# Optimization experiments

Measured on AMD Instinct MI355X. Metric: run time of the kernel, lower is better.

The kernel has to match this reference:

```python
import jax, jax.numpy as jnp
import numpy as np

B, C, CI, H, W = 8, 256, 128, 48, 48


def conv1x1(x, w, b):
    # x: (B,C,H,W), w: (CI,C), b: (CI,)
    return jnp.einsum('bchw,oc->bohw', x, w) + b[None, :, None, None]


def setup_inputs() -> dict:
    key = jax.random.key(0)
    ks = jax.random.split(key, 14)
    s = 1.0 / np.sqrt(C)
    d = {
        'x_1': jax.random.normal(ks[0], (B, C, H, W), jnp.float32),
        'x_2': jax.random.normal(ks[1], (B, C, H, W), jnp.float32),
    }
    names = ['v1', 'k1', 'q1', 'v2', 'k2', 'q2']
    for i, n in enumerate(names):
        d['w_' + n] = jax.random.uniform(ks[2 + 2 * i], (CI, C), jnp.float32, -s, s)
        d['b_' + n] = jax.random.uniform(ks[3 + 2 * i], (CI,), jnp.float32, -s, s)
    return d


def reference(x_1, x_2, w_v1, b_v1, w_k1, b_k1, w_q1, b_q1,
              w_v2, b_v2, w_k2, b_k2, w_q2, b_q2):
    b, ci, h, w = x_1.shape[0], w_v1.shape[0], x_1.shape[2], x_1.shape[3]
    n = h * w
    V1 = conv1x1(x_1, w_v1, b_v1).reshape(b, ci, n)
    K1 = conv1x1(x_1, w_k1, b_k1).reshape(b, ci, n)
    Q1 = conv1x1(x_1, w_q1, b_q1).reshape(b, ci, n)
    V2 = conv1x1(x_2, w_v2, b_v2).reshape(b, ci, n)
    K2 = conv1x1(x_2, w_k2, b_k2).reshape(b, ci, n)
    Q2 = conv1x1(x_2, w_q2, b_q2).reshape(b, ci, n)
    # sigmoid-gated cross attention, (B, N, N)
    R12 = jax.nn.sigmoid(jnp.einsum('bcn,bcm->bnm', Q1, K2))
    R21 = jax.nn.sigmoid(jnp.einsum('bcn,bcm->bnm', Q2, K1))
    Fu1 = jnp.einsum('bnm,bcm->bcn', R12, V2).reshape(b, ci, h, w)
    Fu2 = jnp.einsum('bnm,bcm->bcn', R21, V1).reshape(b, ci, h, w)
    y_1 = jnp.concatenate([x_1, Fu1], axis=1)
    y_2 = jnp.concatenate([x_2, Fu2], axis=1)
    return (y_1, y_2)
```

## Files before the change

kernel.cpp:

```cpp
#include <hip/hip_runtime.h>
#include <hip/hip_bf16.h>


typedef __bf16 bf16;
typedef __bf16 bf16x8 __attribute__((ext_vector_type(8)));
typedef __bf16 bf16x4 __attribute__((ext_vector_type(4)));
typedef float f32x4 __attribute__((ext_vector_type(4)));
typedef float f32x16 __attribute__((ext_vector_type(16)));
typedef unsigned int u32x4 __attribute__((ext_vector_type(4)));

#define NB 8
#define NC 256
#define NCI 128
#define NHW 2304
#define NT32 72

__global__ __launch_bounds__(256) void wconv_kernel(
    const float* __restrict__ w0, const float* __restrict__ w1,
    const float* __restrict__ w2, const float* __restrict__ w3,
    const float* __restrict__ w4, const float* __restrict__ w5,
    bf16* __restrict__ dst)
{
    int idx = (blockIdx.x * 256 + threadIdx.x) * 8;
    int m = idx >> 15;
    int off = idx & 32767;
    const float* w = (m == 0) ? w0 : (m == 1) ? w1 : (m == 2) ? w2
                   : (m == 3) ? w3 : (m == 4) ? w4 : w5;
    f32x4 a0 = *(const f32x4*)(w + off);
    f32x4 a1 = *(const f32x4*)(w + off + 4);
    bf16x8 o;
    #pragma unroll
    for (int j = 0; j < 4; ++j) { o[j] = (bf16)a0[j]; o[4 + j] = (bf16)a1[j]; }
    *(bf16x8*)(dst + idx) = o;
}

__global__ __launch_bounds__(256) void qkv_kernel(
    const float* __restrict__ x1, const float* __restrict__ x2,
    const bf16* __restrict__ wb,
    const float* __restrict__ bv1, const float* __restrict__ bk1, const float* __restrict__ bq1,
    const float* __restrict__ bv2, const float* __restrict__ bk2, const float* __restrict__ bq2,
    bf16* __restrict__ Qt, bf16* __restrict__ Kt, bf16* __restrict__ Vt,
    float* __restrict__ out)
{
    __shared__ __align__(16) bf16 Xt[32 * 264];

    int gid = blockIdx.x;
    int nt = gid % NT32;
    int s = (gid / NT32) & 1;
    int b = gid / (2 * NT32);
    int n0 = nt * 32;

    const float* x = s ? x2 : x1;
    const bf16* wv = wb + (size_t)(s * 3 + 0) * (NCI * NC);
    const bf16* wk = wb + (size_t)(s * 3 + 1) * (NCI * NC);
    const bf16* wq = wb + (size_t)(s * 3 + 2) * (NCI * NC);
    const float* bv = s ? bv2 : bv1;
    const float* bk = s ? bk2 : bk1;
    const float* bq = s ? bq2 : bq1;
    float* outy = out + (size_t)s * (NB * 384 * NHW);

    int tid = threadIdx.x;
    {
        int n_off = (tid & 3) * 8;
        int c0l = tid >> 2;
        #pragma unroll
        for (int i = 0; i < 4; ++i) {
            int c = c0l + i * 64;
            const float* src = x + ((size_t)(b * NC + c) * NHW + n0 + n_off);
            f32x4 a0 = *(const f32x4*)src;
            f32x4 a1 = *(const f32x4*)(src + 4);
            float* dsty = outy + ((size_t)(b * 384 + c) * NHW + n0 + n_off);
            *(f32x4*)dsty = a0;
            *(f32x4*)(dsty + 4) = a1;
            #pragma unroll
            for (int j = 0; j < 4; ++j) {
                Xt[(n_off + j) * 264 + c] = (bf16)a0[j];
                Xt[(n_off + 4 + j) * 264 + c] = (bf16)a1[j];
            }
        }
    }
    __syncthreads();

    int lane = tid & 63;
    int wid = tid >> 6;
    int row = lane & 15, quad = lane >> 4;
    int ci_base = wid * 32;

    f32x4 acc[3][2][2];
    #pragma unroll
    for (int t = 0; t < 3; ++t)
        #pragma unroll
        for (int mi = 0; mi < 2; ++mi)
            #pragma unroll
            for (int j = 0; j < 2; ++j)
                acc[t][mi][j] = (f32x4){0.f, 0.f, 0.f, 0.f};

    const bf16* wptr[3] = {wq, wk, wv};
    #pragma unroll
    for (int ks = 0; ks < 8; ++ks) {
        int c0 = ks * 32 + quad * 8;
        bf16x8 bfrag[2];
        #pragma unroll
        for (int j = 0; j < 2; ++j)
            bfrag[j] = *(const bf16x8*)&Xt[(j * 16 + row) * 264 + c0];
        #pragma unroll
        for (int t = 0; t < 3; ++t) {
            #pragma unroll
            for (int mi = 0; mi < 2; ++mi) {
                bf16x8 afrag = *(const bf16x8*)&wptr[t][(size_t)(ci_base + mi * 16 + row) * NC + c0];
                #pragma unroll
                for (int j = 0; j < 2; ++j)
                    acc[t][mi][j] = __builtin_amdgcn_mfma_f32_16x16x32_bf16(
                        afrag, bfrag[j], acc[t][mi][j], 0, 0, 0);
            }
        }
    }

    size_t qkbase = ((size_t)s * NB + b) * NHW * NCI;
    size_t vbase  = ((size_t)s * NB + b) * NCI * NHW;
    #pragma unroll
    for (int mi = 0; mi < 2; ++mi) {
        int ci0 = ci_base + mi * 16 + quad * 4;
        f32x4 bq4 = *(const f32x4*)&bq[ci0];
        f32x4 bk4 = *(const f32x4*)&bk[ci0];
        f32x4 bv4 = *(const f32x4*)&bv[ci0];
        #pragma unroll
        for (int j = 0; j < 2; ++j) {
            int n = n0 + j * 16 + row;
            bf16x4 pk;
            #pragma unroll
            for (int r = 0; r < 4; ++r) pk[r] = (bf16)(acc[0][mi][j][r] + bq4[r]);
            *(bf16x4*)&Qt[qkbase + (size_t)n * NCI + ci0] = pk;
            #pragma unroll
            for (int r = 0; r < 4; ++r) pk[r] = (bf16)(acc[1][mi][j][r] + bk4[r]);
            *(bf16x4*)&Kt[qkbase + (size_t)n * NCI + ci0] = pk;
            #pragma unroll
            for (int r = 0; r < 4; ++r)
                Vt[vbase + (size_t)(nt * 128 + ci0 + r) * 32 + (j * 16 + row)] =
                    (bf16)(acc[2][mi][j][r] + bv4[r]);
        }
    }
}

__global__ __launch_bounds__(256, 3) void attn_kernel(
    const bf16* __restrict__ Qt, const bf16* __restrict__ Kt, const bf16* __restrict__ Vt,
    float* __restrict__ out)
{
    __shared__ __align__(16) float RED[8192];

    int gid = blockIdx.x;
    int b = gid & 7;
    int dir = (gid >> 3) & 1;
    int nt = gid >> 4;

    int tid = threadIdx.x;
    int lane = tid & 63;
    int mq = tid >> 6;
    int col = lane & 31, hi = lane >> 5;

    int sq = dir, skv = dir ^ 1;
    const bf16* q = Qt + ((size_t)sq  * NB + b) * (NHW * NCI);
    const bf16* k = Kt + ((size_t)skv * NB + b) * (NHW * NCI);
    const bf16* v = Vt + ((size_t)skv * NB + b) * (NCI * NHW);
    float* outy = out + (size_t)dir * (NB * 384 * NHW) + ((size_t)b * 384 + 256) * NHW;

    int nw = nt * 32;

    bf16x8 qf[8];
    #pragma unroll
    for (int j = 0; j < 8; ++j)
        qf[j] = *(const bf16x8*)&q[(size_t)(nw + col) * NCI + j * 16 + hi * 8];

    f32x16 o0, o1, o2, o3;
    #pragma unroll
    for (int j = 0; j < 16; ++j) { o0[j] = 0.f; o1[j] = 0.f; o2[j] = 0.f; o3[j] = 0.f; }

    for (int i = 0; i < 18; ++i) {
        int m0 = mq * 576 + i * 32;
        const bf16* kp = k + (size_t)(m0 + col) * NCI + hi * 8;

        f32x16 s;
        #pragma unroll
        for (int j = 0; j < 16; ++j) s[j] = 0.f;
        __builtin_amdgcn_s_setprio(1);
        #pragma unroll
        for (int j = 0; j < 8; ++j) {
            bf16x8 kf = *(const bf16x8*)(kp + j * 16);
            s = __builtin_amdgcn_mfma_f32_32x32x16_bf16(kf, qf[j], s, 0, 0, 0);
        }
        __builtin_amdgcn_s_setprio(0);

        #pragma unroll
        for (int r = 0; r < 16; ++r) {
            float e = __expf(-s[r]);
            s[r] = __builtin_amdgcn_rcpf(1.0f + e);
        }
        u32x4 pbw0, pbw1;
        {
            unsigned int a0, a1, c0, c1;
            asm("v_cvt_pk_bf16_f32 %0, %1, %2" : "=v"(a0) : "v"(s[0]), "v"(s[1]));
            asm("v_cvt_pk_bf16_f32 %0, %1, %2" : "=v"(a1) : "v"(s[2]), "v"(s[3]));
            asm("v_cvt_pk_bf16_f32 %0, %1, %2" : "=v"(c0) : "v"(s[4]), "v"(s[5]));
            asm("v_cvt_pk_bf16_f32 %0, %1, %2" : "=v"(c1) : "v"(s[6]), "v"(s[7]));
            asm volatile("v_permlane32_swap_b32 %0, %1" : "+v"(a0), "+v"(c0));
            asm volatile("v_permlane32_swap_b32 %0, %1" : "+v"(a1), "+v"(c1));
            pbw0 = (u32x4){a0, a1, c0, c1};
        }
        {
            unsigned int a0, a1, c0, c1;
            asm("v_cvt_pk_bf16_f32 %0, %1, %2" : "=v"(a0) : "v"(s[8]),  "v"(s[9]));
            asm("v_cvt_pk_bf16_f32 %0, %1, %2" : "=v"(a1) : "v"(s[10]), "v"(s[11]));
            asm("v_cvt_pk_bf16_f32 %0, %1, %2" : "=v"(c0) : "v"(s[12]), "v"(s[13]));
            asm("v_cvt_pk_bf16_f32 %0, %1, %2" : "=v"(c1) : "v"(s[14]), "v"(s[15]));
            asm volatile("v_permlane32_swap_b32 %0, %1" : "+v"(a0), "+v"(c0));
            asm volatile("v_permlane32_swap_b32 %0, %1" : "+v"(a1), "+v"(c1));
            pbw1 = (u32x4){a0, a1, c0, c1};
        }

        const bf16* vp = v + ((size_t)(mq * 18 + i) * 128 + col) * 32 + hi * 8;
        __builtin_amdgcn_s_setprio(1);
        {
            bf16x8 pf = __builtin_bit_cast(bf16x8, pbw0);
            o0 = __builtin_amdgcn_mfma_f32_32x32x16_bf16(*(const bf16x8*)(vp + 0*1024), pf, o0, 0, 0, 0);
            o1 = __builtin_amdgcn_mfma_f32_32x32x16_bf16(*(const bf16x8*)(vp + 1*1024), pf, o1, 0, 0, 0);
            o2 = __builtin_amdgcn_mfma_f32_32x32x16_bf16(*(const bf16x8*)(vp + 2*1024), pf, o2, 0, 0, 0);
            o3 = __builtin_amdgcn_mfma_f32_32x32x16_bf16(*(const bf16x8*)(vp + 3*1024), pf, o3, 0, 0, 0);
        }
        {
            bf16x8 pf = __builtin_bit_cast(bf16x8, pbw1);
            o0 = __builtin_amdgcn_mfma_f32_32x32x16_bf16(*(const bf16x8*)(vp + 0*1024 + 16), pf, o0, 0, 0, 0);
            o1 = __builtin_amdgcn_mfma_f32_32x32x16_bf16(*(const bf16x8*)(vp + 1*1024 + 16), pf, o1, 0, 0, 0);
            o2 = __builtin_amdgcn_mfma_f32_32x32x16_bf16(*(const bf16x8*)(vp + 2*1024 + 16), pf, o2, 0, 0, 0);
            o3 = __builtin_amdgcn_mfma_f32_32x32x16_bf16(*(const bf16x8*)(vp + 3*1024 + 16), pf, o3, 0, 0, 0);
        }
        __builtin_amdgcn_s_setprio(0);
    }

    float* buf0 = RED;
    float* buf1 = RED + 4096;

    auto wpart = [&](float* buf, const f32x16& a, int cb) {
        #pragma unroll
        for (int g = 0; g < 4; ++g) {
            f32x4 v4;
            #pragma unroll
            for (int j = 0; j < 4; ++j) v4[j] = a[g * 4 + j];
            *(f32x4*)&buf[lane * 64 + (((cb * 4 + g) ^ (lane & 15)) * 4)] = v4;
        }
    };
    auto rpart = [&](float* buf, f32x16& a, int cb) {
        #pragma unroll
        for (int g = 0; g < 4; ++g) {
            f32x4 v4 = *(const f32x4*)&buf[lane * 64 + (((cb * 4 + g) ^ (lane & 15)) * 4)];
            #pragma unroll
            for (int j = 0; j < 4; ++j) a[g * 4 + j] += v4[j];
        }
    };

    __syncthreads();
    if (mq == 2) { wpart(buf0, o0, 0); wpart(buf0, o1, 1); wpart(buf0, o2, 2); wpart(buf0, o3, 3); }
    if (mq == 3) { wpart(buf1, o0, 0); wpart(buf1, o1, 1); wpart(buf1, o2, 2); wpart(buf1, o3, 3); }
    __syncthreads();
    if (mq == 0) { rpart(buf0, o0, 0); rpart(buf0, o1, 1); rpart(buf0, o2, 2); rpart(buf0, o3, 3); }
    if (mq == 1) { rpart(buf1, o0, 0); rpart(buf1, o1, 1); rpart(buf1, o2, 2); rpart(buf1, o3, 3); }
    __syncthreads();
    if (mq == 1) { wpart(buf0, o0, 0); wpart(buf0, o1, 1); wpart(buf0, o2, 2); wpart(buf0, o3, 3); }
    __syncthreads();
    if (mq == 0) {
        rpart(buf0, o0, 0); rpart(buf0, o1, 1); rpart(buf0, o2, 2); rpart(buf0, o3, 3);
        #pragma unroll
        for (int r = 0; r < 16; ++r) {
            int cr = (r & 3) + 8 * (r >> 2) + 4 * hi;
            outy[(size_t)(0 * 32 + cr) * NHW + nw + col] = o0[r];
            outy[(size_t)(1 * 32 + cr) * NHW + nw + col] = o1[r];
            outy[(size_t)(2 * 32 + cr) * NHW + nw + col] = o2[r];
            outy[(size_t)(3 * 32 + cr) * NHW + nw + col] = o3[r];
        }
    }
}

extern "C" void kernel_launch(void* const* d_in, const int* in_sizes, int n_in,
                              void* d_out, int out_size, void* d_ws, size_t ws_size,
                              hipStream_t stream) {
    const float* x1  = (const float*)d_in[0];
    const float* x2  = (const float*)d_in[1];
    const float* wv1 = (const float*)d_in[2];  const float* bv1 = (const float*)d_in[3];
    const float* wk1 = (const float*)d_in[4];  const float* bk1 = (const float*)d_in[5];
    const float* wq1 = (const float*)d_in[6];  const float* bq1 = (const float*)d_in[7];
    const float* wv2 = (const float*)d_in[8];  const float* bv2 = (const float*)d_in[9];
    const float* wk2 = (const float*)d_in[10]; const float* bk2 = (const float*)d_in[11];
    const float* wq2 = (const float*)d_in[12]; const float* bq2 = (const float*)d_in[13];
    float* out = (float*)d_out;

    size_t per = (size_t)2 * NB * NHW * NCI;
    bf16* Qt = (bf16*)d_ws;
    bf16* Kt = Qt + per;
    bf16* Vt = Kt + per;
    bf16* wb = Vt + per;

    wconv_kernel<<<dim3(96), dim3(256), 0, stream>>>(wv1, wk1, wq1, wv2, wk2, wq2, wb);

    qkv_kernel<<<dim3(NB * 2 * NT32), dim3(256), 0, stream>>>(
        x1, x2, wb, bv1, bk1, bq1, bv2, bk2, bq2, Qt, Kt, Vt, out);

    attn_kernel<<<dim3(NB * 2 * NT32), dim3(256), 0, stream>>>(Qt, Kt, Vt, out);
}
```

Before: 288.9 us.

## Software-pipeline K fragment loads with register double buffering in attention kernel

Restructures the attention loop so that the next tile's K fragments are prefetched into a second register buffer while the current tile is processed. V fragments are loaded at the start of each iteration, ahead of the sigmoid step. The loop is manually unrolled by two to ping-pong the buffers. This raises register pressure, so the occupancy hint is lowered from 3 to 2 blocks per CU, trading wave-level latency hiding for in-wave overlap.

```diff
diff --git a/kernel.cpp b/kernel.cpp
--- a/kernel.cpp
+++ b/kernel.cpp
@@ -142,7 +142,7 @@
     }
 }
 
-__global__ __launch_bounds__(256, 3) void attn_kernel(
+__global__ __launch_bounds__(256, 2) void attn_kernel(
     const bf16* __restrict__ Qt, const bf16* __restrict__ Kt, const bf16* __restrict__ Vt,
     float* __restrict__ out)
 {
@@ -175,19 +175,33 @@
     #pragma unroll
     for (int j = 0; j < 16; ++j) { o0[j] = 0.f; o1[j] = 0.f; o2[j] = 0.f; o3[j] = 0.f; }
 
-    for (int i = 0; i < 18; ++i) {
-        int m0 = mq * 576 + i * 32;
-        const bf16* kp = k + (size_t)(m0 + col) * NCI + hi * 8;
+    const bf16* kbase = k + (size_t)(mq * 576 + col) * NCI + hi * 8;
+    const bf16* vbase = v + ((size_t)(mq * 18) * 128 + col) * 32 + hi * 8;
+
+    bf16x8 kfA[8], kfB[8];
+    #pragma unroll
+    for (int j = 0; j < 8; ++j) kfA[j] = *(const bf16x8*)(kbase + j * 16);
+
+    auto body = [&](bf16x8 (&cur)[8], bf16x8 (&nxt)[8], int i) {
+        const bf16* vp = vbase + (size_t)i * 4096;
+        bf16x8 vf[8];
+        #pragma unroll
+        for (int ct = 0; ct < 4; ++ct) {
+            vf[2 * ct]     = *(const bf16x8*)(vp + ct * 1024);
+            vf[2 * ct + 1] = *(const bf16x8*)(vp + ct * 1024 + 16);
+        }
+        int inx = (i + 1 < 18) ? (i + 1) : 0;
+        const bf16* kpn = kbase + (size_t)inx * 32 * NCI;
+        #pragma unroll
+        for (int j = 0; j < 8; ++j) nxt[j] = *(const bf16x8*)(kpn + j * 16);
 
         f32x16 s;
         #pragma unroll
         for (int j = 0; j < 16; ++j) s[j] = 0.f;
         __builtin_amdgcn_s_setprio(1);
         #pragma unroll
-        for (int j = 0; j < 8; ++j) {
-            bf16x8 kf = *(const bf16x8*)(kp + j * 16);
-            s = __builtin_amdgcn_mfma_f32_32x32x16_bf16(kf, qf[j], s, 0, 0, 0);
-        }
+        for (int j = 0; j < 8; ++j)
+            s = __builtin_amdgcn_mfma_f32_32x32x16_bf16(cur[j], qf[j], s, 0, 0, 0);
         __builtin_amdgcn_s_setprio(0);
 
         #pragma unroll
@@ -217,23 +231,28 @@
             pbw1 = (u32x4){a0, a1, c0, c1};
         }
 
-        const bf16* vp = v + ((size_t)(mq * 18 + i) * 128 + col) * 32 + hi * 8;
         __builtin_amdgcn_s_setprio(1);
         {
             bf16x8 pf = __builtin_bit_cast(bf16x8, pbw0);
-            o0 = __builtin_amdgcn_mfma_f32_32x32x16_bf16(*(const bf16x8*)(vp + 0*1024), pf, o0, 0, 0, 0);
-            o1 = __builtin_amdgcn_mfma_f32_32x32x16_bf16(*(const bf16x8*)(vp + 1*1024), pf, o1, 0, 0, 0);
-            o2 = __builtin_amdgcn_mfma_f32_32x32x16_bf16(*(const bf16x8*)(vp + 2*1024), pf, o2, 0, 0, 0);
-            o3 = __builtin_amdgcn_mfma_f32_32x32x16_bf16(*(const bf16x8*)(vp + 3*1024), pf, o3, 0, 0, 0);
+            o0 = __builtin_amdgcn_mfma_f32_32x32x16_bf16(vf[0], pf, o0, 0, 0, 0);
+            o1 = __builtin_amdgcn_mfma_f32_32x32x16_bf16(vf[2], pf, o1, 0, 0, 0);
+            o2 = __builtin_amdgcn_mfma_f32_32x32x16_bf16(vf[4], pf, o2, 0, 0, 0);
+            o3 = __builtin_amdgcn_mfma_f32_32x32x16_bf16(vf[6], pf, o3, 0, 0, 0);
         }
         {
             bf16x8 pf = __builtin_bit_cast(bf16x8, pbw1);
-            o0 = __builtin_amdgcn_mfma_f32_32x32x16_bf16(*(const bf16x8*)(vp + 0*1024 + 16), pf, o0, 0, 0, 0);
-            o1 = __builtin_amdgcn_mfma_f32_32x32x16_bf16(*(const bf16x8*)(vp + 1*1024 + 16), pf, o1, 0, 0, 0);
-            o2 = __builtin_amdgcn_mfma_f32_32x32x16_bf16(*(const bf16x8*)(vp + 2*1024 + 16), pf, o2, 0, 0, 0);
-            o3 = __builtin_amdgcn_mfma_f32_32x32x16_bf16(*(const bf16x8*)(vp + 3*1024 + 16), pf, o3, 0, 0, 0);
+            o0 = __builtin_amdgcn_mfma_f32_32x32x16_bf16(vf[1], pf, o0, 0, 0, 0);
+            o1 = __builtin_amdgcn_mfma_f32_32x32x16_bf16(vf[3], pf, o1, 0, 0, 0);
+            o2 = __builtin_amdgcn_mfma_f32_32x32x16_bf16(vf[5], pf, o2, 0, 0, 0);
+            o3 = __builtin_amdgcn_mfma_f32_32x32x16_bf16(vf[7], pf, o3, 0, 0, 0);
         }
         __builtin_amdgcn_s_setprio(0);
+    };
+
+    #pragma unroll 1
+    for (int ii = 0; ii < 9; ++ii) {
+        body(kfA, kfB, 2 * ii);
+        body(kfB, kfA, 2 * ii + 1);
     }
 
     float* buf0 = RED;
```

Measured after the change: 284.5 us. Within noise of the previous version (-1.5%).
